# Optimization experiments

Measured on AMD Instinct MI355X. Metric: run time of the kernel, lower is better.

## Reference

```python
import math
import jax, jax.numpy as jnp
import numpy as np

N, M = 2048, 128            # fine grid points, coarse points
IN_NF, H, LMAX = 256, 128, 2
A2B = 1.88973
MIN_STD = 0.32 * A2B / 2.0  # two stddevs reach min covalent radius (Bohr)
MAX_STD = 2.32 * A2B / 2.0


def _sph_lmax2(d):
    # norm-normalized real spherical harmonics (e3nn convention), unit input d[..., 3]
    x, y, z = d[..., 0], d[..., 1], d[..., 2]
    s3 = math.sqrt(3.0)
    sh0 = jnp.ones_like(x)[..., None]                                    # [., 1]
    sh1 = jnp.stack([x, y, z], axis=-1)                                  # [., 3]
    sh2 = jnp.stack([s3 * x * z, s3 * x * y,
                     y * y - 0.5 * (x * x + z * z),
                     s3 * y * z, 0.5 * s3 * (z * z - x * x)], axis=-1)   # [., 5]
    return [sh0, sh1, sh2]


def _radial(dist, nb):
    # Gaussian radial basis; two stddevs span [MIN_COV_RAD, MAX_COV_RAD]
    s = jnp.linspace(MIN_STD, MAX_STD, nb, dtype=dist.dtype)
    temps = 2.0 * s * s
    x2 = dist[..., None] ** 2
    return jnp.exp(-x2 / temps) * (2.0 / 3.0) * x2 / temps / (math.pi * temps) ** 1.5


def setup_inputs():
    key = jax.random.key(0)
    k = jax.random.split(key, 10)
    xav = math.sqrt(6.0 / (H + H))
    return {
        'h': jax.random.normal(k[0], (N, IN_NF), jnp.float32),
        'grid_coords': jax.random.normal(k[1], (N, 3), jnp.float32),
        'coarse_coords': jax.random.normal(k[2], (M, 3), jnp.float32),
        'grid_weights': jax.random.uniform(k[3], (N,), jnp.float32),
        'W_pre': jax.random.normal(k[4], (IN_NF, H), jnp.float32) * math.sqrt(2.0 / (IN_NF + H)),
        'b_pre': jnp.zeros((H,), jnp.float32),
        'W_down': jax.random.uniform(k[5], (LMAX + 1, H, H), jnp.float32, -xav, xav),
        'W_up': jax.random.uniform(k[6], (LMAX + 1, H, H), jnp.float32, -xav, xav),
        'W_post': jax.random.normal(k[7], (H, H), jnp.float32) * math.sqrt(2.0 / (H + H)),
        'b_post': jnp.zeros((H,), jnp.float32),
    }


def reference(h, grid_coords, coarse_coords, grid_weights,
              W_pre, b_pre, W_down, W_up, W_post, b_post):
    h = jax.nn.silu(h @ W_pre + b_pre)                            # [N, H]
    # all-pairs directions/distances (vect_cdist); radius_cutoff = inf -> every pair is an edge
    dvec = grid_coords[:, None, :] - coarse_coords[None, :, :]    # [N, M, 3]
    dist = jnp.sqrt((dvec * dvec + 1e-20).sum(-1))                # [N, M]
    dirs = dvec / dist[..., None]
    sh = _sph_lmax2(dirs)                                         # list of [N, M, 2l+1]
    rad = _radial(dist, H)                                        # [N, M, H]
    # tp_down: paths (0e x le -> le); l=0 uses the scalar branch (no 1/sqrt(2l+1))
    # radial gating per hidden channel + quadrature integration onto coarse nodes
    coarse = []
    for l in range(LMAX + 1):
        norm = 1.0 if l == 0 else math.sqrt(2 * l + 1)
        c = jnp.einsum('nu,uw,nmj,nmw,n->mwj',
                       h, W_down[l], sh[l], rad, grid_weights) / norm
        coarse.append(c)                                          # [M, H, 2l+1]
    # tp_up: paths (le x le -> 0e); l>0 branch divides by sqrt(2l+1); scatter back to grid
    out = 0.0
    for l in range(LMAX + 1):
        norm = 1.0 if l == 0 else math.sqrt(2 * l + 1)
        out = out + jnp.einsum('mui,uw,nmi->nw', coarse[l], W_up[l], sh[l]) / norm
    return jax.nn.silu(out @ W_post + b_post)                     # [N, H]
```

## Files before the change

kernel.cpp:

```cpp
#include <hip/hip_runtime.h>
#include <math.h>

#define N_PTS 2048
#define M_PTS 128
#define INNF  256
#define H     128

#define MIN_STDC 0.30235680f
#define MAX_STDC 2.19208680f
#define PI_F     3.14159265358979f
#define LOG2E_F  1.44269504089f

static __device__ __forceinline__ float silu_f(float x) {
  return x / (1.0f + __expf(-x));
}

__global__ __launch_bounds__(256) void k_sh(const float* __restrict__ gc,
                                            const float* __restrict__ cc,
                                            float* __restrict__ SH) {
  int p = blockIdx.x * 256 + threadIdx.x;
  int n = p >> 7, m = p & 127;
  float gx = gc[3*n], gy = gc[3*n+1], gz = gc[3*n+2];
  float cx = cc[3*m], cy = cc[3*m+1], cz = cc[3*m+2];
  float dx = gx - cx, dy = gy - cy, dz = gz - cz;
  float d2 = dx*dx + dy*dy + dz*dz + 3e-20f;
  float inv = rsqrtf(d2);
  float x = dx*inv, y = dy*inv, z = dz*inv;
  const float s3 = 1.73205080757f;
  float4 q0 = make_float4(1.0f, x, y, z);
  float4 q1 = make_float4(s3*x*z, s3*x*y, y*y - 0.5f*(x*x + z*z), s3*y*z);
  float4 q2 = make_float4(0.5f*s3*(z*z - x*x), d2, 0.0f, 0.0f);
  float4* dst = (float4*)(SH + (size_t)p * 12);
  dst[0] = q0; dst[1] = q1; dst[2] = q2;
}

__global__ __launch_bounds__(256) void k_pre(const float* __restrict__ h,
    const float* __restrict__ W_pre, const float* __restrict__ b_pre,
    const float* __restrict__ W_down, const float* __restrict__ gw,
    float* __restrict__ hdg4) {
  __shared__ float h_lds[4 * INNF];
  __shared__ float hp_lds[4 * H];
  int t = threadIdx.x;
  int n0 = blockIdx.x * 4;
  int w  = t & 127;
  int nh = t >> 7;

  {
    int row = t >> 6, col = (t & 63) << 2;
    float4 v = *(const float4*)(h + (size_t)(n0 + row) * INNF + col);
    *(float4*)&h_lds[row * INNF + col] = v;
  }
  __syncthreads();

  float acc[2] = {0.0f, 0.0f};
  for (int u = 0; u < INNF; u += 4) {
    float4 a0 = *(const float4*)&h_lds[(nh*2 + 0) * INNF + u];
    float4 a1 = *(const float4*)&h_lds[(nh*2 + 1) * INNF + u];
    float w0 = W_pre[(u+0)*H + w];
    float w1 = W_pre[(u+1)*H + w];
    float w2 = W_pre[(u+2)*H + w];
    float w3 = W_pre[(u+3)*H + w];
    acc[0] += a0.x*w0 + a0.y*w1 + a0.z*w2 + a0.w*w3;
    acc[1] += a1.x*w0 + a1.y*w1 + a1.z*w2 + a1.w*w3;
  }
  float bb = b_pre[w];
  hp_lds[(nh*2 + 0)*H + w] = silu_f(acc[0] + bb);
  hp_lds[(nh*2 + 1)*H + w] = silu_f(acc[1] + bb);
  __syncthreads();

  const float stp = (MAX_STDC - MIN_STDC) / 127.0f;
  float s = MIN_STDC + (float)w * stp;
  float temps = 2.0f * s * s;
  float coef = (2.0f/3.0f) / (temps * powf(PI_F * temps, 1.5f));
  float gwv[2] = {gw[n0 + nh*2], gw[n0 + nh*2 + 1]};
  const float invn[3] = {1.0f, 0.57735026919f, 0.44721359550f};

  float a2[3][2] = {};
  for (int u = 0; u < H; u += 4) {
    float4 p0 = *(const float4*)&hp_lds[(nh*2 + 0)*H + u];
    float4 p1 = *(const float4*)&hp_lds[(nh*2 + 1)*H + u];
    #pragma unroll
    for (int l = 0; l < 3; ++l) {
      float w0 = W_down[((size_t)l*H + u + 0)*H + w];
      float w1 = W_down[((size_t)l*H + u + 1)*H + w];
      float w2 = W_down[((size_t)l*H + u + 2)*H + w];
      float w3 = W_down[((size_t)l*H + u + 3)*H + w];
      a2[l][0] += p0.x*w0 + p0.y*w1 + p0.z*w2 + p0.w*w3;
      a2[l][1] += p1.x*w0 + p1.y*w1 + p1.z*w2 + p1.w*w3;
    }
  }
  #pragma unroll
  for (int r = 0; r < 2; ++r) {
    float sc = gwv[r] * coef;
    size_t base = ((size_t)(n0 + nh*2 + r) * H + w) * 4;
    hdg4[base + 0] = a2[0][0+0]*0.0f + a2[0][r]*sc;
    hdg4[base + 1] = a2[1][r]*sc*invn[1];
    hdg4[base + 2] = a2[2][r]*sc*invn[2];
    hdg4[base + 3] = 0.0f;
  }
}

__global__ __launch_bounds__(256) void k_down(const float* __restrict__ gc,
    const float* __restrict__ cc, const float* __restrict__ hdg4,
    float* __restrict__ c_part) {
  __shared__ float lds[4608];
  int t = threadIdx.x;
  int m0 = blockIdx.x * 4;
  int ss = blockIdx.y;
  int n0 = ss * 64;
  int w  = t & 127;
  int nh = t >> 7;

  {
    int n_loc = t >> 2, m_loc = t & 3;
    int n = n0 + n_loc, m = m0 + m_loc;
    float dx = gc[3*n]   - cc[3*m];
    float dy = gc[3*n+1] - cc[3*m+1];
    float dz = gc[3*n+2] - cc[3*m+2];
    float d2 = dx*dx + dy*dy + dz*dz + 3e-20f;
    float inv = rsqrtf(d2);
    float x = dx*inv, y = dy*inv, z = dz*inv;
    const float s3 = 1.73205080757f;
    float* dst = &lds[(size_t)t * 12];
    dst[0] = 1.0f; dst[1] = x; dst[2] = y; dst[3] = z;
    dst[4] = s3*x*z; dst[5] = s3*x*y; dst[6] = y*y - 0.5f*(x*x + z*z);
    dst[7] = s3*y*z; dst[8] = 0.5f*s3*(z*z - x*x);
    dst[9] = d2; dst[10] = 0.0f; dst[11] = 0.0f;
  }
  __syncthreads();

  const float stp = (MAX_STDC - MIN_STDC) / 127.0f;
  float sw = MIN_STDC + (float)w * stp;
  float nl2t = LOG2E_F / (2.0f * sw * sw);

  float acc[4][9] = {};
  for (int j = 0; j < 32; j += 2) {
    int nA = nh*32 + j, nB = nA + 1;
    float4 hA = *(const float4*)(hdg4 + ((size_t)(n0 + nA)*H + w)*4);
    float4 hB = *(const float4*)(hdg4 + ((size_t)(n0 + nB)*H + w)*4);
    #pragma unroll
    for (int half = 0; half < 2; ++half) {
      int nl = half ? nB : nA;
      float4 hv = half ? hB : hA;
      const float* shb = &lds[(size_t)nl * 48];
      #pragma unroll
      for (int mm = 0; mm < 4; ++mm) {
        float4 q0 = *(const float4*)(shb + mm*12);
        float4 q1 = *(const float4*)(shb + mm*12 + 4);
        float4 q2 = *(const float4*)(shb + mm*12 + 8);
        float e  = exp2f(-q2.y * nl2t);
        float rp = e * q2.y;
        float t0 = hv.x*rp, t1 = hv.y*rp, t2 = hv.z*rp;
        acc[mm][0] += t0;
        acc[mm][1] += t1*q0.y; acc[mm][2] += t1*q0.z; acc[mm][3] += t1*q0.w;
        acc[mm][4] += t2*q1.x; acc[mm][5] += t2*q1.y;
        acc[mm][6] += t2*q1.z; acc[mm][7] += t2*q1.w;
        acc[mm][8] += t2*q2.x;
      }
    }
  }

  __syncthreads();
  if (nh == 1) {
    #pragma unroll
    for (int mm = 0; mm < 4; ++mm)
      #pragma unroll
      for (int li = 0; li < 9; ++li)
        lds[(mm*9 + li)*128 + w] = acc[mm][li];
  }
  __syncthreads();
  if (nh == 0) {
    #pragma unroll
    for (int mm = 0; mm < 4; ++mm)
      #pragma unroll
      for (int li = 0; li < 9; ++li) {
        float v = acc[mm][li] + lds[(mm*9 + li)*128 + w];
        c_part[(((size_t)ss*M_PTS + m0 + mm)*9 + li)*H + w] = v;
      }
  }
}

__global__ __launch_bounds__(256) void k_cu(const float* __restrict__ c_part,
    const float* __restrict__ W_up, float* __restrict__ CU) {
  __shared__ float c_lds[H * 12];
  __shared__ float red[9 * H];
  int t = threadIdx.x, m = blockIdx.x;
  int w = t & 127, uh = t >> 7;

  for (int idx = t; idx < 9 * H; idx += 256) {
    int li = idx >> 7, u = idx & 127;
    float v = 0.0f;
    #pragma unroll 8
    for (int s = 0; s < 32; ++s)
      v += c_part[(((size_t)s*M_PTS + m)*9 + li)*H + u];
    c_lds[u*12 + li] = v;
  }
  __syncthreads();

  float acc[9] = {};
  for (int u = uh*64; u < uh*64 + 64; ++u) {
    float4 q0 = *(const float4*)&c_lds[u*12];
    float4 q1 = *(const float4*)&c_lds[u*12 + 4];
    float  q8 = c_lds[u*12 + 8];
    float w0 = W_up[((size_t)0*H + u)*H + w];
    float w1 = W_up[((size_t)1*H + u)*H + w];
    float w2 = W_up[((size_t)2*H + u)*H + w];
    acc[0] += q0.x*w0;
    acc[1] += q0.y*w1; acc[2] += q0.z*w1; acc[3] += q0.w*w1;
    acc[4] += q1.x*w2; acc[5] += q1.y*w2; acc[6] += q1.z*w2;
    acc[7] += q1.w*w2; acc[8] += q8*w2;
  }
  __syncthreads();
  if (uh == 1) {
    #pragma unroll
    for (int li = 0; li < 9; ++li) red[li*128 + w] = acc[li];
  }
  __syncthreads();
  if (uh == 0) {
    const float invn[3] = {1.0f, 0.57735026919f, 0.44721359550f};
    #pragma unroll
    for (int li = 0; li < 9; ++li) {
      int l = (li == 0) ? 0 : (li < 4 ? 1 : 2);
      CU[((size_t)m*12 + li)*H + w] = (acc[li] + red[li*128 + w]) * invn[l];
    }
    #pragma unroll
    for (int li = 9; li < 12; ++li)
      CU[((size_t)m*12 + li)*H + w] = 0.0f;
  }
}

__global__ __launch_bounds__(256) void k_up(const float* __restrict__ SH,
    const float* __restrict__ CU, float* __restrict__ out_part) {
  __shared__ float At[32 * 65];
  __shared__ float Bl[32 * 128];
  int t = threadIdx.x;
  int n0 = blockIdx.x * 64;
  int ks = blockIdx.y;
  int tgn = t >> 4, tgw = t & 15;
  float acc[4][8] = {};
  for (int ch = 0; ch < 3; ++ch) {
    int kc = ks*96 + ch*32;
    #pragma unroll
    for (int i = 0; i < 2; ++i) {
      int idx = t + i*256;
      int n = idx >> 3, q = (idx & 7) << 2;
      float4 v = *(const float4*)(SH + (size_t)(n0 + n)*1536 + kc + q);
      At[(q+0)*65 + n] = v.x; At[(q+1)*65 + n] = v.y;
      At[(q+2)*65 + n] = v.z; At[(q+3)*65 + n] = v.w;
    }
    #pragma unroll
    for (int i = 0; i < 4; ++i) {
      int idx = t + i*256;
      int k = idx >> 5, q = (idx & 31) << 2;
      *(float4*)&Bl[k*128 + q] = *(const float4*)(CU + (size_t)(kc + k)*H + q);
    }
    __syncthreads();
    #pragma unroll 4
    for (int k = 0; k < 32; ++k) {
      float4 a4 = *(const float4*)&At[k*65 + 4*tgn];
      float4 b0 = *(const float4*)&Bl[k*128 + 8*tgw];
      float4 b1 = *(const float4*)&Bl[k*128 + 8*tgw + 4];
      float av[4] = {a4.x, a4.y, a4.z, a4.w};
      float bvv[8] = {b0.x, b0.y, b0.z, b0.w, b1.x, b1.y, b1.z, b1.w};
      #pragma unroll
      for (int r = 0; r < 4; ++r)
        #pragma unroll
        for (int c = 0; c < 8; ++c)
          acc[r][c] += av[r] * bvv[c];
    }
    __syncthreads();
  }
  #pragma unroll
  for (int r = 0; r < 4; ++r) {
    size_t row = (size_t)ks*N_PTS + n0 + 4*tgn + r;
    *(float4*)(out_part + row*H + 8*tgw)     = make_float4(acc[r][0], acc[r][1], acc[r][2], acc[r][3]);
    *(float4*)(out_part + row*H + 8*tgw + 4) = make_float4(acc[r][4], acc[r][5], acc[r][6], acc[r][7]);
  }
}

__global__ __launch_bounds__(256) void k_post(const float* __restrict__ out_part,
    const float* __restrict__ W_post, const float* __restrict__ b_post,
    float* __restrict__ out) {
  __shared__ float op[4 * H];
  int t = threadIdx.x;
  int n0 = blockIdx.x * 4;
  int w = t & 127, nh = t >> 7;

  #pragma unroll
  for (int i = 0; i < 2; ++i) {
    int idx = t + i*256;
    int nl = idx >> 7, ww = idx & 127;
    float v = 0.0f;
    #pragma unroll
    for (int s = 0; s < 16; ++s)
      v += out_part[((size_t)s*N_PTS + n0 + nl)*H + ww];
    op[nl*H + ww] = v;
  }
  __syncthreads();

  float acc[2] = {0.0f, 0.0f};
  for (int u = 0; u < H; u += 4) {
    float4 p0 = *(const float4*)&op[(nh*2 + 0)*H + u];
    float4 p1 = *(const float4*)&op[(nh*2 + 1)*H + u];
    float w0 = W_post[(u+0)*H + w];
    float w1 = W_post[(u+1)*H + w];
    float w2 = W_post[(u+2)*H + w];
    float w3 = W_post[(u+3)*H + w];
    acc[0] += p0.x*w0 + p0.y*w1 + p0.z*w2 + p0.w*w3;
    acc[1] += p1.x*w0 + p1.y*w1 + p1.z*w2 + p1.w*w3;
  }
  float bp = b_post[w];
  out[(size_t)(n0 + nh*2 + 0)*H + w] = silu_f(acc[0] + bp);
  out[(size_t)(n0 + nh*2 + 1)*H + w] = silu_f(acc[1] + bp);
}

extern "C" void kernel_launch(void* const* d_in, const int* in_sizes, int n_in,
                              void* d_out, int out_size, void* d_ws, size_t ws_size,
                              hipStream_t stream) {
  const float* h      = (const float*)d_in[0];
  const float* gc     = (const float*)d_in[1];
  const float* cc     = (const float*)d_in[2];
  const float* gw     = (const float*)d_in[3];
  const float* W_pre  = (const float*)d_in[4];
  const float* b_pre  = (const float*)d_in[5];
  const float* W_down = (const float*)d_in[6];
  const float* W_up   = (const float*)d_in[7];
  const float* W_post = (const float*)d_in[8];
  const float* b_post = (const float*)d_in[9];

  float* ws       = (float*)d_ws;
  float* SH       = ws;
  float* hdg4     = SH + 3145728;
  float* c_part   = hdg4 + 1048576;
  float* CU       = c_part + 4718592;
  float* out_part = c_part;
  float* out      = (float*)d_out;

  k_sh  <<<1024,          256, 0, stream>>>(gc, cc, SH);
  k_pre <<<512,           256, 0, stream>>>(h, W_pre, b_pre, W_down, gw, hdg4);
  k_down<<<dim3(32,32),   256, 0, stream>>>(gc, cc, hdg4, c_part);
  k_cu  <<<128,           256, 0, stream>>>(c_part, W_up, CU);
  k_up  <<<dim3(32,16),   256, 0, stream>>>(SH, CU, out_part);
  k_post<<<512,           256, 0, stream>>>(out_part, W_post, b_post, out);
}
```

Baseline: 161.8 us.

## Fuse spherical-harmonic computation into k_up and drop padded SH buffer

```diff
diff --git a/kernel.cpp b/kernel.cpp
--- a/kernel.cpp
+++ b/kernel.cpp
@@ -13,25 +13,6 @@
 
 static __device__ __forceinline__ float silu_f(float x) {
   return x / (1.0f + __expf(-x));
-}
-
-__global__ __launch_bounds__(256) void k_sh(const float* __restrict__ gc,
-                                            const float* __restrict__ cc,
-                                            float* __restrict__ SH) {
-  int p = blockIdx.x * 256 + threadIdx.x;
-  int n = p >> 7, m = p & 127;
-  float gx = gc[3*n], gy = gc[3*n+1], gz = gc[3*n+2];
-  float cx = cc[3*m], cy = cc[3*m+1], cz = cc[3*m+2];
-  float dx = gx - cx, dy = gy - cy, dz = gz - cz;
-  float d2 = dx*dx + dy*dy + dz*dz + 3e-20f;
-  float inv = rsqrtf(d2);
-  float x = dx*inv, y = dy*inv, z = dz*inv;
-  const float s3 = 1.73205080757f;
-  float4 q0 = make_float4(1.0f, x, y, z);
-  float4 q1 = make_float4(s3*x*z, s3*x*y, y*y - 0.5f*(x*x + z*z), s3*y*z);
-  float4 q2 = make_float4(0.5f*s3*(z*z - x*x), d2, 0.0f, 0.0f);
-  float4* dst = (float4*)(SH + (size_t)p * 12);
-  dst[0] = q0; dst[1] = q1; dst[2] = q2;
 }
 
 __global__ __launch_bounds__(256) void k_pre(const float* __restrict__ h,
@@ -53,15 +34,18 @@
   __syncthreads();
 
   float acc[2] = {0.0f, 0.0f};
-  for (int u = 0; u < INNF; u += 4) {
-    float4 a0 = *(const float4*)&h_lds[(nh*2 + 0) * INNF + u];
-    float4 a1 = *(const float4*)&h_lds[(nh*2 + 1) * INNF + u];
-    float w0 = W_pre[(u+0)*H + w];
-    float w1 = W_pre[(u+1)*H + w];
-    float w2 = W_pre[(u+2)*H + w];
-    float w3 = W_pre[(u+3)*H + w];
-    acc[0] += a0.x*w0 + a0.y*w1 + a0.z*w2 + a0.w*w3;
-    acc[1] += a1.x*w0 + a1.y*w1 + a1.z*w2 + a1.w*w3;
+  for (int u = 0; u < INNF; u += 8) {
+    float4 a0a = *(const float4*)&h_lds[(nh*2 + 0) * INNF + u];
+    float4 a0b = *(const float4*)&h_lds[(nh*2 + 0) * INNF + u + 4];
+    float4 a1a = *(const float4*)&h_lds[(nh*2 + 1) * INNF + u];
+    float4 a1b = *(const float4*)&h_lds[(nh*2 + 1) * INNF + u + 4];
+    float wv[8];
+    #pragma unroll
+    for (int i = 0; i < 8; ++i) wv[i] = W_pre[(u + i)*H + w];
+    acc[0] += a0a.x*wv[0] + a0a.y*wv[1] + a0a.z*wv[2] + a0a.w*wv[3]
+            + a0b.x*wv[4] + a0b.y*wv[5] + a0b.z*wv[6] + a0b.w*wv[7];
+    acc[1] += a1a.x*wv[0] + a1a.y*wv[1] + a1a.z*wv[2] + a1a.w*wv[3]
+            + a1b.x*wv[4] + a1b.y*wv[5] + a1b.z*wv[6] + a1b.w*wv[7];
   }
   float bb = b_pre[w];
   hp_lds[(nh*2 + 0)*H + w] = silu_f(acc[0] + bb);
@@ -73,7 +57,7 @@
   float temps = 2.0f * s * s;
   float coef = (2.0f/3.0f) / (temps * powf(PI_F * temps, 1.5f));
   float gwv[2] = {gw[n0 + nh*2], gw[n0 + nh*2 + 1]};
-  const float invn[3] = {1.0f, 0.57735026919f, 0.44721359550f};
+  const float invn1 = 0.57735026919f, invn2 = 0.44721359550f;
 
   float a2[3][2] = {};
   for (int u = 0; u < H; u += 4) {
@@ -93,9 +77,9 @@
   for (int r = 0; r < 2; ++r) {
     float sc = gwv[r] * coef;
     size_t base = ((size_t)(n0 + nh*2 + r) * H + w) * 4;
-    hdg4[base + 0] = a2[0][0+0]*0.0f + a2[0][r]*sc;
-    hdg4[base + 1] = a2[1][r]*sc*invn[1];
-    hdg4[base + 2] = a2[2][r]*sc*invn[2];
+    hdg4[base + 0] = a2[0][r]*sc;
+    hdg4[base + 1] = a2[1][r]*sc*invn1;
+    hdg4[base + 2] = a2[2][r]*sc*invn2;
     hdg4[base + 3] = 0.0f;
   }
 }
@@ -134,15 +118,14 @@
   float nl2t = LOG2E_F / (2.0f * sw * sw);
 
   float acc[4][9] = {};
-  for (int j = 0; j < 32; j += 2) {
-    int nA = nh*32 + j, nB = nA + 1;
-    float4 hA = *(const float4*)(hdg4 + ((size_t)(n0 + nA)*H + w)*4);
-    float4 hB = *(const float4*)(hdg4 + ((size_t)(n0 + nB)*H + w)*4);
-    #pragma unroll
-    for (int half = 0; half < 2; ++half) {
-      int nl = half ? nB : nA;
-      float4 hv = half ? hB : hA;
-      const float* shb = &lds[(size_t)nl * 48];
+  for (int j = 0; j < 32; j += 4) {
+    float4 hv[4];
+    #pragma unroll
+    for (int q = 0; q < 4; ++q)
+      hv[q] = *(const float4*)(hdg4 + ((size_t)(n0 + nh*32 + j + q)*H + w)*4);
+    #pragma unroll
+    for (int q = 0; q < 4; ++q) {
+      const float* shb = &lds[(size_t)(nh*32 + j + q) * 48];
       #pragma unroll
       for (int mm = 0; mm < 4; ++mm) {
         float4 q0 = *(const float4*)(shb + mm*12);
@@ -150,7 +133,7 @@
         float4 q2 = *(const float4*)(shb + mm*12 + 8);
         float e  = exp2f(-q2.y * nl2t);
         float rp = e * q2.y;
-        float t0 = hv.x*rp, t1 = hv.y*rp, t2 = hv.z*rp;
+        float t0 = hv[q].x*rp, t1 = hv[q].y*rp, t2 = hv[q].z*rp;
         acc[mm][0] += t0;
         acc[mm][1] += t1*q0.y; acc[mm][2] += t1*q0.z; acc[mm][3] += t1*q0.w;
         acc[mm][4] += t2*q1.x; acc[mm][5] += t2*q1.y;
@@ -181,7 +164,7 @@
 }
 
 __global__ __launch_bounds__(256) void k_cu(const float* __restrict__ c_part,
-    const float* __restrict__ W_up, float* __restrict__ CU) {
+    const float* __restrict__ W_up, float* __restrict__ CU9) {
   __shared__ float c_lds[H * 12];
   __shared__ float red[9 * H];
   int t = threadIdx.x, m = blockIdx.x;
@@ -221,60 +204,69 @@
     #pragma unroll
     for (int li = 0; li < 9; ++li) {
       int l = (li == 0) ? 0 : (li < 4 ? 1 : 2);
-      CU[((size_t)m*12 + li)*H + w] = (acc[li] + red[li*128 + w]) * invn[l];
-    }
-    #pragma unroll
-    for (int li = 9; li < 12; ++li)
-      CU[((size_t)m*12 + li)*H + w] = 0.0f;
-  }
-}
-
-__global__ __launch_bounds__(256) void k_up(const float* __restrict__ SH,
-    const float* __restrict__ CU, float* __restrict__ out_part) {
-  __shared__ float At[32 * 65];
-  __shared__ float Bl[32 * 128];
+      CU9[((size_t)m*9 + li)*H + w] = (acc[li] + red[li*128 + w]) * invn[l];
+    }
+  }
+}
+
+__global__ __launch_bounds__(256) void k_up(const float* __restrict__ gc,
+    const float* __restrict__ cc, const float* __restrict__ CU9,
+    float* __restrict__ out_part) {
+  __shared__ float At[36 * 34];
+  __shared__ float Bl[36 * 128];
   int t = threadIdx.x;
-  int n0 = blockIdx.x * 64;
+  int n0 = blockIdx.x * 32;
   int ks = blockIdx.y;
-  int tgn = t >> 4, tgw = t & 15;
-  float acc[4][8] = {};
-  for (int ch = 0; ch < 3; ++ch) {
-    int kc = ks*96 + ch*32;
-    #pragma unroll
-    for (int i = 0; i < 2; ++i) {
+  int tgn = t >> 4;
+  int w0 = (t & 15) * 8;
+  float acc[2][8] = {};
+
+  for (int ch = 0; ch < 2; ++ch) {
+    int m0 = ks*8 + ch*4;
+    __syncthreads();
+    if (t < 128) {
+      int n_loc = t >> 2, m_loc = t & 3;
+      int n = n0 + n_loc, m = m0 + m_loc;
+      float dx = gc[3*n]   - cc[3*m];
+      float dy = gc[3*n+1] - cc[3*m+1];
+      float dz = gc[3*n+2] - cc[3*m+2];
+      float d2 = dx*dx + dy*dy + dz*dz + 3e-20f;
+      float inv = rsqrtf(d2);
+      float x = dx*inv, y = dy*inv, z = dz*inv;
+      const float s3 = 1.73205080757f;
+      float sh[9];
+      sh[0] = 1.0f; sh[1] = x; sh[2] = y; sh[3] = z;
+      sh[4] = s3*x*z; sh[5] = s3*x*y; sh[6] = y*y - 0.5f*(x*x + z*z);
+      sh[7] = s3*y*z; sh[8] = 0.5f*s3*(z*z - x*x);
+      #pragma unroll
+      for (int li = 0; li < 9; ++li)
+        At[(m_loc*9 + li)*34 + n_loc] = sh[li];
+    }
+    #pragma unroll
+    for (int i = 0; i < 5; ++i) {
       int idx = t + i*256;
-      int n = idx >> 3, q = (idx & 7) << 2;
-      float4 v = *(const float4*)(SH + (size_t)(n0 + n)*1536 + kc + q);
-      At[(q+0)*65 + n] = v.x; At[(q+1)*65 + n] = v.y;
-      At[(q+2)*65 + n] = v.z; At[(q+3)*65 + n] = v.w;
-    }
-    #pragma unroll
-    for (int i = 0; i < 4; ++i) {
-      int idx = t + i*256;
-      int k = idx >> 5, q = (idx & 31) << 2;
-      *(float4*)&Bl[k*128 + q] = *(const float4*)(CU + (size_t)(kc + k)*H + q);
+      if (idx < 1152)
+        *(float4*)&Bl[idx*4] = *(const float4*)(CU9 + ((size_t)m0*9)*H + idx*4);
     }
     __syncthreads();
-    #pragma unroll 4
-    for (int k = 0; k < 32; ++k) {
-      float4 a4 = *(const float4*)&At[k*65 + 4*tgn];
-      float4 b0 = *(const float4*)&Bl[k*128 + 8*tgw];
-      float4 b1 = *(const float4*)&Bl[k*128 + 8*tgw + 4];
-      float av[4] = {a4.x, a4.y, a4.z, a4.w};
-      float bvv[8] = {b0.x, b0.y, b0.z, b0.w, b1.x, b1.y, b1.z, b1.w};
-      #pragma unroll
-      for (int r = 0; r < 4; ++r)
-        #pragma unroll
-        for (int c = 0; c < 8; ++c)
-          acc[r][c] += av[r] * bvv[c];
-    }
-    __syncthreads();
+    #pragma unroll 6
+    for (int k = 0; k < 36; ++k) {
+      float2 a = *(const float2*)&At[k*34 + 2*tgn];
+      float4 b0 = *(const float4*)&Bl[k*128 + w0];
+      float4 b1 = *(const float4*)&Bl[k*128 + w0 + 4];
+      float bv[8] = {b0.x, b0.y, b0.z, b0.w, b1.x, b1.y, b1.z, b1.w};
+      #pragma unroll
+      for (int c = 0; c < 8; ++c) {
+        acc[0][c] += a.x * bv[c];
+        acc[1][c] += a.y * bv[c];
+      }
+    }
   }
   #pragma unroll
-  for (int r = 0; r < 4; ++r) {
-    size_t row = (size_t)ks*N_PTS + n0 + 4*tgn + r;
-    *(float4*)(out_part + row*H + 8*tgw)     = make_float4(acc[r][0], acc[r][1], acc[r][2], acc[r][3]);
-    *(float4*)(out_part + row*H + 8*tgw + 4) = make_float4(acc[r][4], acc[r][5], acc[r][6], acc[r][7]);
+  for (int r = 0; r < 2; ++r) {
+    size_t row = (size_t)ks*N_PTS + n0 + 2*tgn + r;
+    *(float4*)(out_part + row*H + w0)     = make_float4(acc[r][0], acc[r][1], acc[r][2], acc[r][3]);
+    *(float4*)(out_part + row*H + w0 + 4) = make_float4(acc[r][4], acc[r][5], acc[r][6], acc[r][7]);
   }
 }
 
@@ -329,17 +321,15 @@
   const float* b_post = (const float*)d_in[9];
 
   float* ws       = (float*)d_ws;
-  float* SH       = ws;
-  float* hdg4     = SH + 3145728;
+  float* hdg4     = ws;
   float* c_part   = hdg4 + 1048576;
-  float* CU       = c_part + 4718592;
+  float* CU9      = c_part + 4718592;
   float* out_part = c_part;
   float* out      = (float*)d_out;
 
-  k_sh  <<<1024,          256, 0, stream>>>(gc, cc, SH);
   k_pre <<<512,           256, 0, stream>>>(h, W_pre, b_pre, W_down, gw, hdg4);
   k_down<<<dim3(32,32),   256, 0, stream>>>(gc, cc, hdg4, c_part);
-  k_cu  <<<128,           256, 0, stream>>>(c_part, W_up, CU);
-  k_up  <<<dim3(32,16),   256, 0, stream>>>(SH, CU, out_part);
+  k_cu  <<<128,           256, 0, stream>>>(c_part, W_up, CU9);
+  k_up  <<<dim3(64,16),   256, 0, stream>>>(gc, cc, CU9, out_part);
   k_post<<<512,           256, 0, stream>>>(out_part, W_post, b_post, out);
 }
```

After: 166.1 us. 1.03x slower.
